# Performance work log

Measured on AMD Instinct MI355X. Metric: run time of the kernel, lower is better.

The kernel has to match this reference:

```python
import jax, jax.numpy as jnp
import numpy as np

DIM = 192
HEADS = 6
WS = (6, 12)          # (lat, lon) window
INPUT_SHAPE = (186, 360)
TOW = INPUT_SHAPE[0] // WS[0]   # 31 latitude window types
N_WIN = WS[0] * WS[1]           # 72 tokens per window


def _position_index():
    """Earth-specific relative-position index (static, numpy)."""
    ws0, ws1 = WS
    coords_hi = np.arange(ws0)
    coords_hj = -np.arange(ws0) * ws0
    coords_w = np.arange(ws1)
    c1 = np.stack(np.meshgrid(coords_hi, coords_w, indexing='ij'))  # (2, ws0, ws1)
    c2 = np.stack(np.meshgrid(coords_hj, coords_w, indexing='ij'))
    f1 = c1.reshape(2, -1)
    f2 = c2.reshape(2, -1)
    coords = f1[:, :, None] - f2[:, None, :]      # (2, N, N)
    coords = coords.transpose(1, 2, 0).copy()     # (N, N, 2)
    coords[:, :, 1] += ws1 - 1                    # shift lon diff to >= 0
    coords[:, :, 0] *= 2 * ws1 - 1                # row stride in bias table
    return jnp.asarray(coords.sum(-1).reshape(-1))  # (N*N,) int


def setup_inputs() -> dict:
    key = jax.random.key(0)
    ks = jax.random.split(key, 6)
    B = 2
    nW = INPUT_SHAPE[1] // WS[1]          # 30
    B_ = B * TOW * nW                     # 1860
    table_rows = (2 * WS[1] - 1) * WS[0] * WS[0]  # 828
    return {
        "x": jax.random.normal(ks[0], (B_, N_WIN, DIM), dtype=jnp.float32),
        "mask": jnp.zeros((nW, N_WIN, N_WIN), dtype=jnp.float32),
        "w_qkv": jax.random.normal(ks[1], (DIM, 3 * DIM), dtype=jnp.float32) * 0.02,
        "b_qkv": jnp.zeros((3 * DIM,), dtype=jnp.float32),
        "w_out": jax.random.normal(ks[2], (DIM, DIM), dtype=jnp.float32) * 0.02,
        "b_out": jnp.zeros((DIM,), dtype=jnp.float32),
        "bias_table": jax.random.normal(ks[3], (table_rows, TOW, HEADS), dtype=jnp.float32) * 0.02,
    }


def reference(x, mask, w_qkv, b_qkv, w_out, b_out, bias_table):
    B_, N, dim = x.shape
    hd = dim // HEADS
    scale = hd ** -0.5
    # fused QKV projection
    qkv = (x @ w_qkv + b_qkv).reshape(B_, N, 3, HEADS, hd)
    qkv = qkv.transpose(2, 0, 3, 1, 4)            # (3, B_, H, N, hd)
    q, k, v = qkv[0] * scale, qkv[1], qkv[2]
    attn = jnp.einsum('bhnd,bhmd->bhnm', q, k)    # (B_, H, N, N)
    # earth-specific bias: gather table rows by relative-position index,
    # tiled across the window batch exactly as the torch code's .repeat()
    rep = B_ // TOW
    pos = _position_index()                       # (N*N,)
    bias = bias_table[jnp.tile(pos, rep)]         # (rep*N*N, TOW, H)
    bias = bias.reshape(N, N, -1, HEADS).transpose(2, 3, 0, 1)  # (B_, H, N, N)
    attn = attn + bias
    # window mask (broadcast over groups of nW lon-windows)
    nW = mask.shape[0]
    attn = attn.reshape(B_ // nW, nW, HEADS, N, N) + mask[None, :, None]
    attn = attn.reshape(B_, HEADS, N, N)
    attn = jax.nn.softmax(attn, axis=-1)          # dropout is identity (p=0 / eval)
    out = jnp.einsum('bhnm,bhmd->bhnd', attn, v)  # (B_, H, N, hd)
    out = out.transpose(0, 2, 1, 3).reshape(B_, N, dim)
    return out @ w_out + b_out
```

## Files before the change

### kernel.cpp

```cpp
#include <hip/hip_runtime.h>
#include <cstddef>

typedef short bf16x8 __attribute__((ext_vector_type(8)));
typedef float f32x4  __attribute__((ext_vector_type(4)));

namespace {
constexpr float QSCALE = 0.17677669529663687f;

constexpr size_t BQKV_OFF = 0;
constexpr size_t WOUT_OFF = 576 * 384 * 2;
constexpr size_t BQG_OFF  = WOUT_OFF + 192 * 384 * 2;
constexpr size_t WS_BYTES = BQG_OFF + 576 * 4;

constexpr int AXS  = 392;
constexpr int AX_H = 0;
constexpr int Q2_H = 72 * AXS;
constexpr int K2_H = Q2_H + 2 * 72 * 40;
constexpr int V2_H = K2_H + 2 * 72 * 40;
constexpr int PB_H = V2_H + 2 * 32 * 104;
constexpr int RM_H = PB_H + 8 * 16 * 104;
constexpr int HALF_TOT = RM_H + 5184;
constexpr int BT_F = HALF_TOT / 2;
constexpr int LDSA_BYTES = HALF_TOT * 2 + 828 * 6 * 4;
}

__device__ __forceinline__ unsigned short f2bf(float f) {
  unsigned int u = __builtin_bit_cast(unsigned int, f);
  return (unsigned short)((u + 0x7FFFu + ((u >> 16) & 1u)) >> 16);
}
__device__ __forceinline__ float bf2f(unsigned short h) {
  unsigned int u = ((unsigned int)h) << 16;
  return __builtin_bit_cast(float, u);
}
__device__ __forceinline__ int moffv(int i) { return (i < 4) ? i * 16 : 56; }

__global__ __launch_bounds__(256)
void prep_kernel(const float* __restrict__ wqkv, const float* __restrict__ bqkv,
                 const float* __restrict__ wout, unsigned char* __restrict__ ws) {
  int t = blockIdx.x * 256 + threadIdx.x;
  unsigned short* Bq = (unsigned short*)(ws + BQKV_OFF);
  unsigned short* Bo = (unsigned short*)(ws + WOUT_OFF);
  float* bqg = (float*)(ws + BQG_OFF);
  if (t < 576 * 384) {
    int n = t / 384, kk = t % 384;
    int ksrc = kk % 192, part = kk / 192;
    int h = n / 96, r96 = n % 96, kind = r96 / 32, d = r96 % 32;
    float w = wqkv[(size_t)ksrc * 576 + kind * 192 + h * 32 + d];
    if (kind == 0) w *= QSCALE;
    unsigned short hi = f2bf(w);
    Bq[t] = part ? f2bf(w - bf2f(hi)) : hi;
  } else if (t < 576 * 384 + 192 * 384) {
    int t2 = t - 576 * 384;
    int n = t2 / 384, kk = t2 % 384, ksrc = kk % 192, part = kk / 192;
    float w = wout[(size_t)ksrc * 192 + n];
    unsigned short hi = f2bf(w);
    Bo[t2] = part ? f2bf(w - bf2f(hi)) : hi;
  } else if (t < 576 * 384 + 192 * 384 + 576) {
    int n = t - (576 * 384 + 192 * 384);
    int h = n / 96, r96 = n % 96, kind = r96 / 32, d = r96 % 32;
    float b = bqkv[kind * 192 + h * 32 + d];
    if (kind == 0) b *= QSCALE;
    bqg[n] = b;
  }
}

template<int NM>
__device__ __forceinline__ void gemm_tiles(const unsigned short* __restrict__ abase_lds,
                                           const unsigned short* __restrict__ bptr,
                                           int m0idx, int lanen, int quad, f32x4* acc) {
  #pragma unroll
  for (int i = 0; i < NM; ++i) acc[i] = (f32x4){0.f, 0.f, 0.f, 0.f};
  #pragma unroll 1
  for (int reg = 0; reg < 3; ++reg) {
    const int ab = (reg == 2) ? 192 : 0;
    const int bb = (reg == 1) ? 192 : 0;
    #pragma unroll 2
    for (int s = 0; s < 6; ++s) {
      bf16x8 bfr = *(const bf16x8*)(bptr + bb + 32 * s);
      #pragma unroll
      for (int mi = 0; mi < NM; ++mi) {
        int mo = moffv(m0idx + mi);
        bf16x8 afr = *(const bf16x8*)(abase_lds + (mo + lanen) * AXS + ab + 32 * s + quad * 8);
        acc[mi] = __builtin_amdgcn_mfma_f32_16x16x32_bf16(afr, bfr, acc[mi], 0, 0, 0);
      }
    }
  }
}

__global__ __launch_bounds__(512)
void attn_kernel(const float* __restrict__ x, const float* __restrict__ mask,
                 const float* __restrict__ btab, const unsigned char* __restrict__ ws,
                 float* __restrict__ out) {
  extern __shared__ unsigned short sm[];
  float* btabs = ((float*)sm) + BT_F;
  unsigned short* rm = sm + RM_H;

  const int w = blockIdx.x, tid = threadIdx.x;
  const int lane = tid & 63, ty = tid >> 6;
  const int lanen = lane & 15, quad = lane >> 4;
  const int mrow = w % 30, tlat = w % 31, w31 = w / 31;
  const float* xw = x + (size_t)w * (72 * 192);
  const float* maskw = mask + (size_t)mrow * (72 * 72);
  const unsigned short* Bq = (const unsigned short*)(ws + BQKV_OFF);
  const float* bqg = (const float*)(ws + BQG_OFF);

  for (int i = tid; i < 3456; i += 512) {
    int r = i / 48, c4 = i % 48;
    float4 v = *(const float4*)(xw + r * 192 + c4 * 4);
    unsigned short h0 = f2bf(v.x), h1 = f2bf(v.y), h2 = f2bf(v.z), h3 = f2bf(v.w);
    ushort4 hv; hv.x = h0; hv.y = h1; hv.z = h2; hv.w = h3;
    ushort4 lv;
    lv.x = f2bf(v.x - bf2f(h0)); lv.y = f2bf(v.y - bf2f(h1));
    lv.z = f2bf(v.z - bf2f(h2)); lv.w = f2bf(v.w - bf2f(h3));
    *(ushort4*)(sm + AX_H + r * AXS + c4 * 4) = hv;
    *(ushort4*)(sm + AX_H + r * AXS + 192 + c4 * 4) = lv;
  }
  for (int i = tid; i < 5184; i += 512) {
    int P = (i * 60 + w31) % 5184;
    int p1 = P / 72, p2 = P % 72;
    int i1 = p1 / 12, j1 = p1 % 12, i2 = p2 / 12, j2 = p2 % 12;
    rm[i] = (unsigned short)((i1 + 6 * i2) * 23 + j1 - j2 + 11);
  }
  for (int i = tid; i < 4968; i += 512)
    btabs[i] = btab[(size_t)(i / 6) * 186 + tlat * 6 + (i % 6)];
  for (int i = tid; i < 9984; i += 512)
    ((unsigned int*)(sm + V2_H))[i] = 0u;
  __syncthreads();

  #pragma unroll 1
  for (int p = 0; p < 3; ++p) {
    const int nbase = 192 * p;

    #pragma unroll 1
    for (int i = 0; i < 3; ++i) {
      int jj = ty + 8 * i;
      int nt = jj % 12, mg = jj / 12;
      const unsigned short* bptr = Bq + (size_t)(nbase + nt * 16 + lanen) * 384 + quad * 8;
      f32x4 acc[3];
      if (mg == 0) gemm_tiles<3>(sm + AX_H, bptr, 0, lanen, quad, acc);
      else         gemm_tiles<2>(sm + AX_H, bptr, 3, lanen, quad, acc);
      float bias = bqg[nbase + nt * 16 + lanen];
      int hh = (nt >= 6), w96 = (nt % 6) * 16;
      int nm = mg ? 2 : 3, m0 = mg ? 3 : 0;
      #pragma unroll
      for (int mi = 0; mi < 3; ++mi) {
        if (mi >= nm) break;
        int mo = moffv(m0 + mi);
        if (w96 < 64) {
          unsigned short* dst = sm + ((w96 < 32) ? Q2_H : K2_H) + hh * 2880;
          int d = (w96 < 32) ? (w96 + lanen) : (w96 - 32 + lanen);
          #pragma unroll
          for (int r = 0; r < 4; ++r)
            dst[(mo + quad * 4 + r) * 40 + d] = f2bf(acc[mi][r] + bias);
        } else {
          int d = w96 - 64 + lanen;
          ushort4 hv;
          hv.x = f2bf(acc[mi][0] + bias); hv.y = f2bf(acc[mi][1] + bias);
          hv.z = f2bf(acc[mi][2] + bias); hv.w = f2bf(acc[mi][3] + bias);
          *(ushort4*)(sm + V2_H + hh * 3328 + d * 104 + mo + quad * 4) = hv;
        }
      }
    }
    __syncthreads();

    #pragma unroll 1
    for (int j = ty; j < 10; j += 8) {
      int hh = j / 5, mo = moffv(j % 5);
      const unsigned short* q2 = sm + Q2_H + hh * 2880;
      const unsigned short* k2 = sm + K2_H + hh * 2880;
      const unsigned short* v2 = sm + V2_H + hh * 3328;
      unsigned short* pb = sm + PB_H + ty * 1664;

      bf16x8 afr = *(const bf16x8*)(q2 + (mo + lanen) * 40 + quad * 8);
      f32x4 s[5];
      #pragma unroll
      for (int t = 0; t < 5; ++t) {
        int no = (t < 4) ? t * 16 : 64;
        bf16x8 bfr = *(const bf16x8*)(k2 + (no + lanen) * 40 + quad * 8);
        s[t] = (f32x4){0.f, 0.f, 0.f, 0.f};
        s[t] = __builtin_amdgcn_mfma_f32_16x16x32_bf16(afr, bfr, s[t], 0, 0, 0);
      }
      int h = 2 * p + hh;
      float lg[5][4];
      #pragma unroll
      for (int t = 0; t < 5; ++t) {
        int ct = ((t < 4) ? t * 16 : 64) + lanen;
        #pragma unroll
        for (int r = 0; r < 4; ++r) {
          if (ct < 72) {
            int m = mo + quad * 4 + r;
            float bv = btabs[(int)rm[m * 72 + ct] * 6 + h];
            lg[t][r] = s[t][r] + bv + maskw[m * 72 + ct];
          } else lg[t][r] = -1e30f;
        }
      }
      #pragma unroll
      for (int r = 0; r < 4; ++r) {
        float mx = fmaxf(fmaxf(fmaxf(lg[0][r], lg[1][r]), fmaxf(lg[2][r], lg[3][r])), lg[4][r]);
        #pragma unroll
        for (int o = 8; o > 0; o >>= 1) mx = fmaxf(mx, __shfl_xor(mx, o));
        float sum = 0.f;
        #pragma unroll
        for (int t = 0; t < 5; ++t) { lg[t][r] = __expf(lg[t][r] - mx); sum += lg[t][r]; }
        #pragma unroll
        for (int o = 8; o > 0; o >>= 1) sum += __shfl_xor(sum, o);
        float inv = 1.0f / sum;
        #pragma unroll
        for (int t = 0; t < 5; ++t) {
          int ct = ((t < 4) ? t * 16 : 64) + lanen;
          if (ct < 72) pb[(quad * 4 + r) * 104 + ct] = f2bf(lg[t][r] * inv);
        }
      }
      f32x4 o2[2];
      o2[0] = (f32x4){0.f, 0.f, 0.f, 0.f}; o2[1] = (f32x4){0.f, 0.f, 0.f, 0.f};
      #pragma unroll
      for (int ks = 0; ks < 3; ++ks) {
        bf16x8 pfr = *(const bf16x8*)(pb + lanen * 104 + ks * 32 + quad * 8);
        #pragma unroll
        for (int n2 = 0; n2 < 2; ++n2) {
          bf16x8 vfr = *(const bf16x8*)(v2 + (n2 * 16 + lanen) * 104 + ks * 32 + quad * 8);
          o2[n2] = __builtin_amdgcn_mfma_f32_16x16x32_bf16(pfr, vfr, o2[n2], 0, 0, 0);
        }
      }
      #pragma unroll
      for (int n2 = 0; n2 < 2; ++n2) {
        int col = h * 32 + n2 * 16 + lanen;
        #pragma unroll
        for (int r = 0; r < 4; ++r)
          out[((size_t)w * 72 + mo + quad * 4 + r) * 192 + col] = o2[n2][r];
      }
    }
    __syncthreads();
  }
}

__global__ __launch_bounds__(256)
void outproj_kernel(const unsigned char* __restrict__ ws, const float* __restrict__ bout,
                    float* __restrict__ out) {
  __shared__ unsigned short Ax[72 * AXS];
  const int w = blockIdx.x, tid = threadIdx.x;
  const int lane = tid & 63, ty = tid >> 6;
  const int lanen = lane & 15, quad = lane >> 4;
  const unsigned short* Bo = (const unsigned short*)(ws + WOUT_OFF);
  float* rows = out + (size_t)w * (72 * 192);

  for (int i = tid; i < 3456; i += 256) {
    int r = i / 48, c4 = i % 48;
    float4 v = *(const float4*)(rows + r * 192 + c4 * 4);
    unsigned short h0 = f2bf(v.x), h1 = f2bf(v.y), h2 = f2bf(v.z), h3 = f2bf(v.w);
    ushort4 hv; hv.x = h0; hv.y = h1; hv.z = h2; hv.w = h3;
    ushort4 lv;
    lv.x = f2bf(v.x - bf2f(h0)); lv.y = f2bf(v.y - bf2f(h1));
    lv.z = f2bf(v.z - bf2f(h2)); lv.w = f2bf(v.w - bf2f(h3));
    *(ushort4*)(Ax + r * AXS + c4 * 4) = hv;
    *(ushort4*)(Ax + r * AXS + 192 + c4 * 4) = lv;
  }
  __syncthreads();

  #pragma unroll 1
  for (int nt = ty; nt < 12; nt += 4) {
    const unsigned short* bptr = Bo + (size_t)(nt * 16 + lanen) * 384 + quad * 8;
    f32x4 acc[5];
    gemm_tiles<5>(Ax, bptr, 0, lanen, quad, acc);
    float bias = bout[nt * 16 + lanen];
    #pragma unroll
    for (int mi = 0; mi < 5; ++mi) {
      int mo = moffv(mi);
      #pragma unroll
      for (int r = 0; r < 4; ++r)
        rows[(mo + quad * 4 + r) * 192 + nt * 16 + lanen] = acc[mi][r] + bias;
    }
  }
}

extern "C" void kernel_launch(void* const* d_in, const int* in_sizes, int n_in,
                              void* d_out, int out_size, void* d_ws, size_t ws_size,
                              hipStream_t stream) {
  const float* x    = (const float*)d_in[0];
  const float* mask = (const float*)d_in[1];
  const float* wqkv = (const float*)d_in[2];
  const float* bqkv = (const float*)d_in[3];
  const float* wout = (const float*)d_in[4];
  const float* bout = (const float*)d_in[5];
  const float* btab = (const float*)d_in[6];
  float* out = (float*)d_out;
  unsigned char* ws = (unsigned char*)d_ws;
  const int nwindows = in_sizes[0] / (72 * 192);

  prep_kernel<<<dim3(1155), dim3(256), 0, stream>>>(wqkv, bqkv, wout, ws);

  (void)hipFuncSetAttribute((const void*)attn_kernel,
                            hipFuncAttributeMaxDynamicSharedMemorySize, LDSA_BYTES);
  attn_kernel<<<dim3(nwindows), dim3(512), LDSA_BYTES, stream>>>(x, mask, btab, ws, out);

  outproj_kernel<<<dim3(nwindows), dim3(256), 0, stream>>>(ws, bout, out);
}
```

Measured before the change: 771.9 us.

## Restructure QKV and out-proj GEMMs for register reuse, reuse LDS, pre-split attn output

```diff
diff --git a/kernel.cpp b/kernel.cpp
--- a/kernel.cpp
+++ b/kernel.cpp
@@ -10,18 +10,15 @@
 constexpr size_t BQKV_OFF = 0;
 constexpr size_t WOUT_OFF = 576 * 384 * 2;
 constexpr size_t BQG_OFF  = WOUT_OFF + 192 * 384 * 2;
-constexpr size_t WS_BYTES = BQG_OFF + 576 * 4;
-
-constexpr int AXS  = 392;
-constexpr int AX_H = 0;
-constexpr int Q2_H = 72 * AXS;
-constexpr int K2_H = Q2_H + 2 * 72 * 40;
-constexpr int V2_H = K2_H + 2 * 72 * 40;
-constexpr int PB_H = V2_H + 2 * 32 * 104;
-constexpr int RM_H = PB_H + 8 * 16 * 104;
-constexpr int HALF_TOT = RM_H + 5184;
-constexpr int BT_F = HALF_TOT / 2;
-constexpr int LDSA_BYTES = HALF_TOT * 2 + 828 * 6 * 4;
+
+constexpr int AXS   = 392;
+constexpr int AX_H  = 0;
+constexpr int Q2A_H = 72 * AXS;
+constexpr int K2A_H = Q2A_H + 6 * 72 * 32;
+constexpr int V2A_H = K2A_H + 6 * 72 * 40;
+constexpr int HALF_TOT = V2A_H + 6 * 32 * 104;
+constexpr int PB_H  = 828 * 6 * 2;
+constexpr int LDSA_BYTES = HALF_TOT * 2;
 }
 
 __device__ __forceinline__ unsigned short f2bf(float f) {
@@ -65,36 +62,76 @@
 }
 
 template<int NM>
-__device__ __forceinline__ void gemm_tiles(const unsigned short* __restrict__ abase_lds,
-                                           const unsigned short* __restrict__ bptr,
-                                           int m0idx, int lanen, int quad, f32x4* acc) {
-  #pragma unroll
-  for (int i = 0; i < NM; ++i) acc[i] = (f32x4){0.f, 0.f, 0.f, 0.f};
+__device__ __forceinline__ void qkv_wave(unsigned short* sm, const unsigned short* __restrict__ Bq,
+                                         const float* __restrict__ bqg, int ntb3, int m0idx,
+                                         int lanen, int quad) {
   #pragma unroll 1
-  for (int reg = 0; reg < 3; ++reg) {
-    const int ab = (reg == 2) ? 192 : 0;
-    const int bb = (reg == 1) ? 192 : 0;
-    #pragma unroll 2
-    for (int s = 0; s < 6; ++s) {
-      bf16x8 bfr = *(const bf16x8*)(bptr + bb + 32 * s);
+  for (int p = 0; p < 3; ++p) {
+    const int nbase = 192 * p;
+    f32x4 acc[3][NM];
+    #pragma unroll
+    for (int nt = 0; nt < 3; ++nt)
+      #pragma unroll
+      for (int mi = 0; mi < NM; ++mi)
+        acc[nt][mi] = (f32x4){0.f, 0.f, 0.f, 0.f};
+    #pragma unroll 1
+    for (int reg = 0; reg < 3; ++reg) {
+      const int ab = (reg == 2) ? 192 : 0;
+      const int bb = (reg == 1) ? 192 : 0;
+      bf16x8 a[NM][6];
       #pragma unroll
       for (int mi = 0; mi < NM; ++mi) {
-        int mo = moffv(m0idx + mi);
-        bf16x8 afr = *(const bf16x8*)(abase_lds + (mo + lanen) * AXS + ab + 32 * s + quad * 8);
-        acc[mi] = __builtin_amdgcn_mfma_f32_16x16x32_bf16(afr, bfr, acc[mi], 0, 0, 0);
-      }
-    }
-  }
-}
-
-__global__ __launch_bounds__(512)
+        const unsigned short* ap = sm + AX_H + (moffv(m0idx + mi) + lanen) * AXS + ab + quad * 8;
+        #pragma unroll
+        for (int s = 0; s < 6; ++s)
+          a[mi][s] = *(const bf16x8*)(ap + 32 * s);
+      }
+      #pragma unroll
+      for (int nt = 0; nt < 3; ++nt) {
+        const unsigned short* bp = Bq + (size_t)(nbase + (ntb3 + nt) * 16 + lanen) * 384 + bb + quad * 8;
+        #pragma unroll
+        for (int s = 0; s < 6; ++s) {
+          bf16x8 bfr = *(const bf16x8*)(bp + 32 * s);
+          #pragma unroll
+          for (int mi = 0; mi < NM; ++mi)
+            acc[nt][mi] = __builtin_amdgcn_mfma_f32_16x16x32_bf16(a[mi][s], bfr, acc[nt][mi], 0, 0, 0);
+        }
+      }
+    }
+    #pragma unroll 1
+    for (int nt = 0; nt < 3; ++nt) {
+      const int ng = ntb3 + nt;
+      const float bias = bqg[nbase + ng * 16 + lanen];
+      const int hh = 2 * p + (ng >= 6 ? 1 : 0);
+      const int w96 = (ng % 6) * 16;
+      #pragma unroll
+      for (int mi = 0; mi < NM; ++mi) {
+        const int mo = moffv(m0idx + mi);
+        if (w96 < 64) {
+          unsigned short* dst;
+          int stride, d;
+          if (w96 < 32) { dst = sm + Q2A_H + hh * 2304; stride = 32; d = w96 + lanen; }
+          else          { dst = sm + K2A_H + hh * 2880; stride = 40; d = w96 - 32 + lanen; }
+          #pragma unroll
+          for (int r = 0; r < 4; ++r)
+            dst[(mo + quad * 4 + r) * stride + d] = f2bf(acc[nt][mi][r] + bias);
+        } else {
+          const int d = w96 - 64 + lanen;
+          ushort4 hv;
+          hv.x = f2bf(acc[nt][mi][0] + bias); hv.y = f2bf(acc[nt][mi][1] + bias);
+          hv.z = f2bf(acc[nt][mi][2] + bias); hv.w = f2bf(acc[nt][mi][3] + bias);
+          *(ushort4*)(sm + V2A_H + hh * 3328 + d * 104 + mo + quad * 4) = hv;
+        }
+      }
+    }
+  }
+}
+
+__global__ __launch_bounds__(512, 2)
 void attn_kernel(const float* __restrict__ x, const float* __restrict__ mask,
                  const float* __restrict__ btab, const unsigned char* __restrict__ ws,
                  float* __restrict__ out) {
   extern __shared__ unsigned short sm[];
-  float* btabs = ((float*)sm) + BT_F;
-  unsigned short* rm = sm + RM_H;
-
   const int w = blockIdx.x, tid = threadIdx.x;
   const int lane = tid & 63, ty = tid >> 6;
   const int lanen = lane & 15, quad = lane >> 4;
@@ -115,126 +152,106 @@
     *(ushort4*)(sm + AX_H + r * AXS + c4 * 4) = hv;
     *(ushort4*)(sm + AX_H + r * AXS + 192 + c4 * 4) = lv;
   }
-  for (int i = tid; i < 5184; i += 512) {
-    int P = (i * 60 + w31) % 5184;
-    int p1 = P / 72, p2 = P % 72;
-    int i1 = p1 / 12, j1 = p1 % 12, i2 = p2 / 12, j2 = p2 % 12;
-    rm[i] = (unsigned short)((i1 + 6 * i2) * 23 + j1 - j2 + 11);
-  }
+  for (int i = tid; i < 9984; i += 512)
+    ((unsigned int*)(sm + V2A_H))[i] = 0u;
+  __syncthreads();
+
+  {
+    const int mg = ty >> 2, ntb3 = (ty & 3) * 3;
+    if (mg == 0) qkv_wave<3>(sm, Bq, bqg, ntb3, 0, lanen, quad);
+    else         qkv_wave<2>(sm, Bq, bqg, ntb3, 3, lanen, quad);
+  }
+  __syncthreads();
+
+  float* btabs = (float*)sm;
   for (int i = tid; i < 4968; i += 512)
     btabs[i] = btab[(size_t)(i / 6) * 186 + tlat * 6 + (i % 6)];
-  for (int i = tid; i < 9984; i += 512)
-    ((unsigned int*)(sm + V2_H))[i] = 0u;
+  for (int i = tid; i < 6656; i += 512)
+    ((unsigned int*)(sm + PB_H))[i] = 0u;
   __syncthreads();
 
+  unsigned short* pb = sm + PB_H + ty * 1664;
+  unsigned short* po = (unsigned short*)(out + (size_t)w * (72 * 192));
   #pragma unroll 1
-  for (int p = 0; p < 3; ++p) {
-    const int nbase = 192 * p;
-
-    #pragma unroll 1
-    for (int i = 0; i < 3; ++i) {
-      int jj = ty + 8 * i;
-      int nt = jj % 12, mg = jj / 12;
-      const unsigned short* bptr = Bq + (size_t)(nbase + nt * 16 + lanen) * 384 + quad * 8;
-      f32x4 acc[3];
-      if (mg == 0) gemm_tiles<3>(sm + AX_H, bptr, 0, lanen, quad, acc);
-      else         gemm_tiles<2>(sm + AX_H, bptr, 3, lanen, quad, acc);
-      float bias = bqg[nbase + nt * 16 + lanen];
-      int hh = (nt >= 6), w96 = (nt % 6) * 16;
-      int nm = mg ? 2 : 3, m0 = mg ? 3 : 0;
-      #pragma unroll
-      for (int mi = 0; mi < 3; ++mi) {
-        if (mi >= nm) break;
-        int mo = moffv(m0 + mi);
-        if (w96 < 64) {
-          unsigned short* dst = sm + ((w96 < 32) ? Q2_H : K2_H) + hh * 2880;
-          int d = (w96 < 32) ? (w96 + lanen) : (w96 - 32 + lanen);
-          #pragma unroll
-          for (int r = 0; r < 4; ++r)
-            dst[(mo + quad * 4 + r) * 40 + d] = f2bf(acc[mi][r] + bias);
-        } else {
-          int d = w96 - 64 + lanen;
-          ushort4 hv;
-          hv.x = f2bf(acc[mi][0] + bias); hv.y = f2bf(acc[mi][1] + bias);
-          hv.z = f2bf(acc[mi][2] + bias); hv.w = f2bf(acc[mi][3] + bias);
-          *(ushort4*)(sm + V2_H + hh * 3328 + d * 104 + mo + quad * 4) = hv;
-        }
-      }
-    }
-    __syncthreads();
-
-    #pragma unroll 1
-    for (int j = ty; j < 10; j += 8) {
-      int hh = j / 5, mo = moffv(j % 5);
-      const unsigned short* q2 = sm + Q2_H + hh * 2880;
-      const unsigned short* k2 = sm + K2_H + hh * 2880;
-      const unsigned short* v2 = sm + V2_H + hh * 3328;
-      unsigned short* pb = sm + PB_H + ty * 1664;
-
-      bf16x8 afr = *(const bf16x8*)(q2 + (mo + lanen) * 40 + quad * 8);
-      f32x4 s[5];
-      #pragma unroll
-      for (int t = 0; t < 5; ++t) {
-        int no = (t < 4) ? t * 16 : 64;
-        bf16x8 bfr = *(const bf16x8*)(k2 + (no + lanen) * 40 + quad * 8);
-        s[t] = (f32x4){0.f, 0.f, 0.f, 0.f};
-        s[t] = __builtin_amdgcn_mfma_f32_16x16x32_bf16(afr, bfr, s[t], 0, 0, 0);
-      }
-      int h = 2 * p + hh;
-      float lg[5][4];
+  for (int j = ty; j < 30; j += 8) {
+    const int hh = j / 5, mo = moffv(j % 5);
+    const unsigned short* q2 = sm + Q2A_H + hh * 2304;
+    const unsigned short* k2 = sm + K2A_H + hh * 2880;
+    const unsigned short* v2 = sm + V2A_H + hh * 3328;
+
+    bf16x8 afr = *(const bf16x8*)(q2 + (mo + lanen) * 32 + quad * 8);
+    f32x4 s[5];
+    #pragma unroll
+    for (int t = 0; t < 5; ++t) {
+      int no = (t < 4) ? t * 16 : 64;
+      bf16x8 bfr = *(const bf16x8*)(k2 + (no + lanen) * 40 + quad * 8);
+      s[t] = (f32x4){0.f, 0.f, 0.f, 0.f};
+      s[t] = __builtin_amdgcn_mfma_f32_16x16x32_bf16(afr, bfr, s[t], 0, 0, 0);
+    }
+    float lg[5][4];
+    #pragma unroll
+    for (int t = 0; t < 5; ++t) {
+      int ct = ((t < 4) ? t * 16 : 64) + lanen;
+      #pragma unroll
+      for (int r = 0; r < 4; ++r) {
+        if (ct < 72) {
+          int m = mo + quad * 4 + r;
+          unsigned int e = (unsigned)(m % 6); e = e ? 6u - e : 0u;
+          unsigned int T = 864u * e + 60u * (unsigned)ct + (unsigned)w31;
+          if (T >= 5184u) T -= 5184u;
+          unsigned int p1 = T / 72u, p2 = T - 72u * p1;
+          unsigned int i1 = p1 / 12u, j1 = p1 - 12u * i1;
+          unsigned int i2 = p2 / 12u, j2 = p2 - 12u * i2;
+          int rowb = (int)((i1 + 6u * i2) * 23u + j1) - (int)j2 + 11;
+          float bv = btabs[rowb * 6 + hh];
+          lg[t][r] = s[t][r] + bv + maskw[m * 72 + ct];
+        } else lg[t][r] = -1e30f;
+      }
+    }
+    #pragma unroll
+    for (int r = 0; r < 4; ++r) {
+      float mx = fmaxf(fmaxf(fmaxf(lg[0][r], lg[1][r]), fmaxf(lg[2][r], lg[3][r])), lg[4][r]);
+      #pragma unroll
+      for (int o = 8; o > 0; o >>= 1) mx = fmaxf(mx, __shfl_xor(mx, o));
+      float sum = 0.f;
+      #pragma unroll
+      for (int t = 0; t < 5; ++t) { lg[t][r] = __expf(lg[t][r] - mx); sum += lg[t][r]; }
+      #pragma unroll
+      for (int o = 8; o > 0; o >>= 1) sum += __shfl_xor(sum, o);
+      float inv = 1.0f / sum;
       #pragma unroll
       for (int t = 0; t < 5; ++t) {
         int ct = ((t < 4) ? t * 16 : 64) + lanen;
-        #pragma unroll
-        for (int r = 0; r < 4; ++r) {
-          if (ct < 72) {
-            int m = mo + quad * 4 + r;
-            float bv = btabs[(int)rm[m * 72 + ct] * 6 + h];
-            lg[t][r] = s[t][r] + bv + maskw[m * 72 + ct];
-          } else lg[t][r] = -1e30f;
-        }
-      }
+        if (ct < 72) pb[(quad * 4 + r) * 104 + ct] = f2bf(lg[t][r] * inv);
+      }
+    }
+    f32x4 o2[2];
+    o2[0] = (f32x4){0.f, 0.f, 0.f, 0.f}; o2[1] = (f32x4){0.f, 0.f, 0.f, 0.f};
+    #pragma unroll
+    for (int ks = 0; ks < 3; ++ks) {
+      bf16x8 pfr = *(const bf16x8*)(pb + lanen * 104 + ks * 32 + quad * 8);
+      #pragma unroll
+      for (int n2 = 0; n2 < 2; ++n2) {
+        bf16x8 vfr = *(const bf16x8*)(v2 + (n2 * 16 + lanen) * 104 + ks * 32 + quad * 8);
+        o2[n2] = __builtin_amdgcn_mfma_f32_16x16x32_bf16(pfr, vfr, o2[n2], 0, 0, 0);
+      }
+    }
+    #pragma unroll
+    for (int n2 = 0; n2 < 2; ++n2) {
+      int col = hh * 32 + n2 * 16 + lanen;
       #pragma unroll
       for (int r = 0; r < 4; ++r) {
-        float mx = fmaxf(fmaxf(fmaxf(lg[0][r], lg[1][r]), fmaxf(lg[2][r], lg[3][r])), lg[4][r]);
-        #pragma unroll
-        for (int o = 8; o > 0; o >>= 1) mx = fmaxf(mx, __shfl_xor(mx, o));
-        float sum = 0.f;
-        #pragma unroll
-        for (int t = 0; t < 5; ++t) { lg[t][r] = __expf(lg[t][r] - mx); sum += lg[t][r]; }
-        #pragma unroll
-        for (int o = 8; o > 0; o >>= 1) sum += __shfl_xor(sum, o);
-        float inv = 1.0f / sum;
-        #pragma unroll
-        for (int t = 0; t < 5; ++t) {
-          int ct = ((t < 4) ? t * 16 : 64) + lanen;
-          if (ct < 72) pb[(quad * 4 + r) * 104 + ct] = f2bf(lg[t][r] * inv);
-        }
-      }
-      f32x4 o2[2];
-      o2[0] = (f32x4){0.f, 0.f, 0.f, 0.f}; o2[1] = (f32x4){0.f, 0.f, 0.f, 0.f};
-      #pragma unroll
-      for (int ks = 0; ks < 3; ++ks) {
-        bf16x8 pfr = *(const bf16x8*)(pb + lanen * 104 + ks * 32 + quad * 8);
-        #pragma unroll
-        for (int n2 = 0; n2 < 2; ++n2) {
-          bf16x8 vfr = *(const bf16x8*)(v2 + (n2 * 16 + lanen) * 104 + ks * 32 + quad * 8);
-          o2[n2] = __builtin_amdgcn_mfma_f32_16x16x32_bf16(pfr, vfr, o2[n2], 0, 0, 0);
-        }
-      }
-      #pragma unroll
-      for (int n2 = 0; n2 < 2; ++n2) {
-        int col = h * 32 + n2 * 16 + lanen;
-        #pragma unroll
-        for (int r = 0; r < 4; ++r)
-          out[((size_t)w * 72 + mo + quad * 4 + r) * 192 + col] = o2[n2][r];
-      }
-    }
-    __syncthreads();
-  }
-}
-
-__global__ __launch_bounds__(256)
+        int row = mo + quad * 4 + r;
+        float v = o2[n2][r];
+        unsigned short hi = f2bf(v);
+        po[row * 384 + col] = hi;
+        po[row * 384 + 192 + col] = f2bf(v - bf2f(hi));
+      }
+    }
+  }
+}
+
+__global__ __launch_bounds__(256, 2)
 void outproj_kernel(const unsigned char* __restrict__ ws, const float* __restrict__ bout,
                     float* __restrict__ out) {
   __shared__ unsigned short Ax[72 * AXS];
@@ -243,32 +260,59 @@
   const int lanen = lane & 15, quad = lane >> 4;
   const unsigned short* Bo = (const unsigned short*)(ws + WOUT_OFF);
   float* rows = out + (size_t)w * (72 * 192);
+  const unsigned short* rw = (const unsigned short*)rows;
 
   for (int i = tid; i < 3456; i += 256) {
-    int r = i / 48, c4 = i % 48;
-    float4 v = *(const float4*)(rows + r * 192 + c4 * 4);
-    unsigned short h0 = f2bf(v.x), h1 = f2bf(v.y), h2 = f2bf(v.z), h3 = f2bf(v.w);
-    ushort4 hv; hv.x = h0; hv.y = h1; hv.z = h2; hv.w = h3;
-    ushort4 lv;
-    lv.x = f2bf(v.x - bf2f(h0)); lv.y = f2bf(v.y - bf2f(h1));
-    lv.z = f2bf(v.z - bf2f(h2)); lv.w = f2bf(v.w - bf2f(h3));
-    *(ushort4*)(Ax + r * AXS + c4 * 4) = hv;
-    *(ushort4*)(Ax + r * AXS + 192 + c4 * 4) = lv;
+    int r = i / 48, c8 = i % 48;
+    *(uint4*)(Ax + r * AXS + c8 * 8) = *(const uint4*)(rw + r * 384 + c8 * 8);
   }
   __syncthreads();
 
+  const int ntb3 = ty * 3;
+  f32x4 acc[3][5];
+  #pragma unroll
+  for (int nt = 0; nt < 3; ++nt)
+    #pragma unroll
+    for (int mi = 0; mi < 5; ++mi)
+      acc[nt][mi] = (f32x4){0.f, 0.f, 0.f, 0.f};
+
   #pragma unroll 1
-  for (int nt = ty; nt < 12; nt += 4) {
-    const unsigned short* bptr = Bo + (size_t)(nt * 16 + lanen) * 384 + quad * 8;
-    f32x4 acc[5];
-    gemm_tiles<5>(Ax, bptr, 0, lanen, quad, acc);
-    float bias = bout[nt * 16 + lanen];
+  for (int reg = 0; reg < 3; ++reg) {
+    const int ab = (reg == 2) ? 192 : 0;
+    const int bb = (reg == 1) ? 192 : 0;
+    #pragma unroll 1
+    for (int hk = 0; hk < 2; ++hk) {
+      bf16x8 a[5][3];
+      #pragma unroll
+      for (int mi = 0; mi < 5; ++mi) {
+        const unsigned short* ap = Ax + (moffv(mi) + lanen) * AXS + ab + hk * 96 + quad * 8;
+        #pragma unroll
+        for (int s2 = 0; s2 < 3; ++s2)
+          a[mi][s2] = *(const bf16x8*)(ap + 32 * s2);
+      }
+      #pragma unroll
+      for (int nt = 0; nt < 3; ++nt) {
+        const unsigned short* bp = Bo + (size_t)((ntb3 + nt) * 16 + lanen) * 384 + bb + hk * 96 + quad * 8;
+        #pragma unroll
+        for (int s2 = 0; s2 < 3; ++s2) {
+          bf16x8 bfr = *(const bf16x8*)(bp + 32 * s2);
+          #pragma unroll
+          for (int mi = 0; mi < 5; ++mi)
+            acc[nt][mi] = __builtin_amdgcn_mfma_f32_16x16x32_bf16(a[mi][s2], bfr, acc[nt][mi], 0, 0, 0);
+        }
+      }
+    }
+  }
+
+  #pragma unroll 1
+  for (int nt = 0; nt < 3; ++nt) {
+    const float bias = bout[(ntb3 + nt) * 16 + lanen];
     #pragma unroll
     for (int mi = 0; mi < 5; ++mi) {
-      int mo = moffv(mi);
+      const int mo = moffv(mi);
       #pragma unroll
       for (int r = 0; r < 4; ++r)
-        rows[(mo + quad * 4 + r) * 192 + nt * 16 + lanen] = acc[mi][r] + bias;
+        rows[(mo + quad * 4 + r) * 192 + (ntb3 + nt) * 16 + lanen] = acc[nt][mi][r] + bias;
     }
   }
 }
```

Result: slower. 820.5 us (+6.3%).
